# Optimization experiments

Measured on AMD Instinct MI355X. Metric: run time of the kernel, lower is better.

Reference implementation:

```python
import jax, jax.numpy as jnp
import numpy as np

B, T, V, NS, L, G, H = 16, 256, 18000, 30, 10, 3, 400


def setup_inputs() -> dict:
    key = jax.random.key(0)
    ks = jax.random.split(key, 12)
    return {
        'encoded_hidden': jax.random.normal(ks[0], (1, B, H), jnp.float32),
        'encoded_outputs': jax.random.normal(ks[1], (B, T, H), jnp.float32),
        'emb_weight': jax.random.normal(ks[2], (V, H), jnp.float32) * 0.02,
        'gru_w_ih': jax.random.normal(ks[3], (3 * H, H), jnp.float32) * 0.05,
        'gru_w_hh': jax.random.normal(ks[4], (3 * H, H), jnp.float32) * 0.05,
        'gru_b_ih': jnp.zeros((3 * H,), jnp.float32),
        'gru_b_hh': jnp.zeros((3 * H,), jnp.float32),
        'w_ratio': jax.random.normal(ks[5], (1, 3 * H), jnp.float32) * 0.05,
        'b_ratio': jnp.zeros((1,), jnp.float32),
        'w_gate': jax.random.normal(ks[6], (G, H), jnp.float32) * 0.05,
        'b_gate': jnp.zeros((G,), jnp.float32),
        'slot_emb': jax.random.normal(ks[7], (2 * NS, H), jnp.float32) * 0.1,
        'encoded_lens': jax.random.randint(ks[8], (B,), T // 2, T + 1, jnp.int32),
        'story': jax.random.randint(ks[9], (B, T), 0, V, jnp.int32),
        'target_batches': jax.random.randint(ks[10], (B, NS, L), 0, V, jnp.int32),
        'domain_idx': 2 * jnp.arange(NS, dtype=jnp.int32),
        'slotname_idx': 2 * jnp.arange(NS, dtype=jnp.int32) + 1,
    }


def _forward(encoded_hidden, encoded_outputs, emb_weight, gru_w_ih, gru_w_hh,
             gru_b_ih, gru_b_hh, w_ratio, b_ratio, w_gate, b_gate, slot_emb,
             encoded_lens, story, target_batches, domain_idx, slotname_idx):
    b, t, h = encoded_outputs.shape
    ns, l = target_batches.shape[1], target_batches.shape[2]
    n = ns * b  # flattened slot-major rows: row = slot*b + batch

    combined = slot_emb[domain_idx] + slot_emb[slotname_idx]          # (NS,H)
    dec_in0 = jnp.repeat(combined, b, axis=0)                          # (N,H)
    h0 = jnp.tile(encoded_hidden[0], (ns, 1))                          # (N,H)
    enc = jnp.tile(encoded_outputs, (ns, 1, 1))                        # (N,T,H)
    story_rep = jnp.tile(story, (ns, 1))                               # (N,T)
    lens_rep = jnp.tile(encoded_lens, ns)                              # (N,)
    mask = jnp.arange(t)[None, :] < lens_rep[:, None]                  # (N,T)
    rows = jnp.arange(n)[:, None]

    # teacher forcing: decoder input at step wi>=1 is emb of target at wi-1
    tgt = jnp.transpose(target_batches, (2, 1, 0)).reshape(l, n)       # (L,N)
    dec_inputs = jnp.concatenate([dec_in0[None], emb_weight[tgt[:-1]]], axis=0)

    def step(hid, x):
        gi = x @ gru_w_ih.T + gru_b_ih
        gh = hid @ gru_w_hh.T + gru_b_hh
        i_r, i_z, i_n = jnp.split(gi, 3, axis=-1)
        h_r, h_z, h_n = jnp.split(gh, 3, axis=-1)
        r = jax.nn.sigmoid(i_r + h_r)
        z = jax.nn.sigmoid(i_z + h_z)
        nn_ = jnp.tanh(i_n + r * h_n)
        h_new = (1.0 - z) * nn_ + z * hid                              # (N,H)
        # attend over encoder outputs
        scores = jnp.einsum('nh,nth->nt', h_new, enc)
        scores = jnp.where(mask, scores, -1e9)
        prob = jax.nn.softmax(scores, axis=1)                          # (N,T)
        context = jnp.einsum('nt,nth->nh', prob, enc)                  # (N,H)
        # vocab distribution
        p_vocab = jax.nn.softmax(h_new @ emb_weight.T, axis=1)         # (N,V)
        # pointer-generator mix
        p_gen_vec = jnp.concatenate([h_new, context, x], axis=-1)      # (N,3H)
        switch = jax.nn.sigmoid(p_gen_vec @ w_ratio.T + b_ratio)       # (N,1)
        p_ctx = jnp.zeros_like(p_vocab).at[rows, story_rep].add(prob)  # scatter-add
        final = (1.0 - switch) * p_ctx + switch * p_vocab              # (N,V)
        return h_new, (final, context)

    _, (finals, contexts) = jax.lax.scan(step, h0, dec_inputs)
    points = finals.reshape(l, ns, b, -1).transpose(1, 2, 0, 3)        # (NS,B,L,V)
    gates = (contexts[0] @ w_gate.T + b_gate).reshape(ns, b, -1)       # (NS,B,G)
    return points, gates


def reference(encoded_hidden, encoded_outputs, emb_weight, gru_w_ih, gru_w_hh,
              gru_b_ih, gru_b_hh, w_ratio, b_ratio, w_gate, b_gate, slot_emb,
              encoded_lens, story, target_batches, domain_idx, slotname_idx):
    return _forward(encoded_hidden, encoded_outputs, emb_weight, gru_w_ih,
                    gru_w_hh, gru_b_ih, gru_b_hh, w_ratio, b_ratio, w_gate,
                    b_gate, slot_emb, encoded_lens, story, target_batches,
                    domain_idx, slotname_idx)
```

## Files before the change

kernel.cpp:

```cpp
#include <hip/hip_runtime.h>
#include <hip/hip_bf16.h>

#define Bq 16
#define Tq 256
#define Vq 18000
#define NSq 30
#define Lq 10
#define Gq 3
#define Hq 400
#define Nq (NSq * Bq)
#define H3q (3 * Hq)
#define CHq 9000

typedef __bf16 bf16;
typedef __bf16 bf16x4 __attribute__((ext_vector_type(4)));
typedef __bf16 bf16x8 __attribute__((ext_vector_type(8)));
typedef float floatx16 __attribute__((ext_vector_type(16)));

__global__ __launch_bounds__(256) void k_f2b4(
    const float* __restrict__ src, bf16* __restrict__ dst, const int n4)
{
    int i = blockIdx.x * 256 + threadIdx.x;
    if (i >= n4) return;
    const float4 v = ((const float4*)src)[i];
    bf16x4 o;
    o[0] = (bf16)v.x; o[1] = (bf16)v.y; o[2] = (bf16)v.z; o[3] = (bf16)v.w;
    ((bf16x4*)dst)[i] = o;
}

__global__ __launch_bounds__(256) void k_prep(
    const float* __restrict__ slot_emb, const int* __restrict__ dom,
    const int* __restrict__ slo, const bf16* __restrict__ embb,
    const int* __restrict__ tgt, const float* __restrict__ ehid,
    float* __restrict__ h, bf16* __restrict__ hb, bf16* __restrict__ xb,
    const int step)
{
    int i = blockIdx.x * 256 + threadIdx.x;
    if (i >= Nq * Hq) return;
    int n = i / Hq, k = i - n * Hq;
    int s = n / Bq, b = n & (Bq - 1);
    if (step == 0) {
        float v = slot_emb[dom[s] * Hq + k] + slot_emb[slo[s] * Hq + k];
        xb[i] = (bf16)v;
        float hv = ehid[b * Hq + k];
        h[i] = hv;
        hb[i] = (bf16)hv;
    } else {
        int tv = tgt[(b * NSq + s) * Lq + (step - 1)];
        xb[i] = embb[(size_t)tv * Hq + k];
    }
}

__global__ __launch_bounds__(256) void k_gru_gemm(
    const bf16* __restrict__ xb, const bf16* __restrict__ hb,
    const bf16* __restrict__ w_ih, const bf16* __restrict__ w_hh,
    float* __restrict__ gi, float* __restrict__ gh)
{
    const int ct = blockIdx.x;
    const int which = blockIdx.z;
    const int wave = threadIdx.x >> 6;
    const int lane = threadIdx.x & 63;
    const int g = blockIdx.y * 4 + wave;
    if (g >= 15) return;
    const bf16* A = which ? hb : xb;
    const bf16* W = which ? w_hh : w_ih;
    float* O = which ? gh : gi;
    const int m = lane & 31;
    const int kh = (lane >> 5) * 8;
    const int row = g * 32 + m;
    int col = ct * 32 + m;
    if (col >= H3q) col = H3q - 1;
    const bf16* Ap = A + row * Hq + kh;
    const bf16* Wp = W + col * Hq + kh;
    floatx16 acc;
    #pragma unroll
    for (int r = 0; r < 16; ++r) acc[r] = 0.f;
    for (int kt = 0; kt < 25; ++kt) {
        bf16x8 a = *(const bf16x8*)(Ap + kt * 16);
        bf16x8 w = *(const bf16x8*)(Wp + kt * 16);
        acc = __builtin_amdgcn_mfma_f32_32x32x16_bf16(a, w, acc, 0, 0, 0);
    }
    const int j = ct * 32 + (lane & 31);
    if (j < H3q) {
        const int rbase = g * 32 + 4 * (lane >> 5);
        #pragma unroll
        for (int r = 0; r < 16; ++r) {
            int rr = rbase + (r & 3) + 8 * (r >> 2);
            O[rr * H3q + j] = acc[r];
        }
    }
}

__global__ __launch_bounds__(256) void k_gru_attn(
    const float* __restrict__ gi, const float* __restrict__ gh,
    const float* __restrict__ b_ih, const float* __restrict__ b_hh,
    float* __restrict__ h, bf16* __restrict__ hb,
    const bf16* __restrict__ xb, const bf16* __restrict__ encb,
    const int* __restrict__ lens, const float* __restrict__ w_ratio,
    const float* __restrict__ b_ratio, const float* __restrict__ w_gate,
    const float* __restrict__ b_gate, float* __restrict__ prob,
    float* __restrict__ swp, float* __restrict__ out_gates, const int step)
{
    const int n = blockIdx.x;
    const int b = n & (Bq - 1);
    const int tid = threadIdx.x;
    __shared__ float s_h[Hq];
    __shared__ float s_c[Hq];
    __shared__ float s_p[Tq];
    __shared__ float s_red[4];

    const float* gin = gi + n * H3q;
    const float* ghn = gh + n * H3q;
    for (int k = tid; k < Hq; k += 256) {
        float ir = gin[k]          + b_ih[k];
        float hr = ghn[k]          + b_hh[k];
        float iz = gin[Hq + k]     + b_ih[Hq + k];
        float hz = ghn[Hq + k]     + b_hh[Hq + k];
        float in_ = gin[2*Hq + k]  + b_ih[2*Hq + k];
        float hn_ = ghn[2*Hq + k]  + b_hh[2*Hq + k];
        float r = 1.f / (1.f + __expf(-(ir + hr)));
        float z = 1.f / (1.f + __expf(-(iz + hz)));
        float nn = tanhf(in_ + r * hn_);
        float hp = h[n * Hq + k];
        float hv = (1.f - z) * nn + z * hp;
        s_h[k] = hv;
        h[n * Hq + k] = hv;
        hb[n * Hq + k] = (bf16)hv;
    }
    __syncthreads();

    const int t = tid;
    const bf16* erow = encb + (size_t)(b * Tq + t) * Hq;
    float sc = 0.f;
    #pragma unroll 5
    for (int kc = 0; kc < Hq / 8; ++kc) {
        bf16x8 e = *(const bf16x8*)(erow + kc * 8);
        #pragma unroll
        for (int j = 0; j < 8; ++j) sc += s_h[kc * 8 + j] * (float)e[j];
    }
    const int len = lens[b];
    float score = (t < len) ? sc : -1e9f;

    float mx = score;
    for (int off = 32; off > 0; off >>= 1) mx = fmaxf(mx, __shfl_xor(mx, off, 64));
    if ((tid & 63) == 0) s_red[tid >> 6] = mx;
    __syncthreads();
    mx = fmaxf(fmaxf(s_red[0], s_red[1]), fmaxf(s_red[2], s_red[3]));
    float ev = __expf(score - mx);
    float sm = ev;
    for (int off = 32; off > 0; off >>= 1) sm += __shfl_xor(sm, off, 64);
    __syncthreads();
    if ((tid & 63) == 0) s_red[tid >> 6] = sm;
    __syncthreads();
    sm = s_red[0] + s_red[1] + s_red[2] + s_red[3];
    float p = ev / sm;
    s_p[t] = p;
    prob[n * Tq + t] = p;
    __syncthreads();

    for (int k = tid; k < Hq; k += 256) {
        float c = 0.f;
        const bf16* ecol = encb + (size_t)b * Tq * Hq + k;
        for (int tt = 0; tt < Tq; ++tt) c += s_p[tt] * (float)ecol[tt * Hq];
        s_c[k] = c;
    }
    __syncthreads();

    float part = 0.f;
    for (int k = tid; k < Hq; k += 256) {
        part += w_ratio[k]        * s_h[k]
              + w_ratio[Hq + k]   * s_c[k]
              + w_ratio[2*Hq + k] * (float)xb[n * Hq + k];
    }
    for (int off = 32; off > 0; off >>= 1) part += __shfl_xor(part, off, 64);
    __syncthreads();
    if ((tid & 63) == 0) s_red[tid >> 6] = part;
    __syncthreads();
    if (tid == 0) {
        float tot = s_red[0] + s_red[1] + s_red[2] + s_red[3] + b_ratio[0];
        swp[n] = 1.f / (1.f + __expf(-tot));
    }

    if (step == 0) {
        for (int gg = 0; gg < Gq; ++gg) {
            float pg = 0.f;
            for (int k = tid; k < Hq; k += 256)
                pg += w_gate[gg * Hq + k] * s_c[k];
            for (int off = 32; off > 0; off >>= 1) pg += __shfl_xor(pg, off, 64);
            __syncthreads();
            if ((tid & 63) == 0) s_red[tid >> 6] = pg;
            __syncthreads();
            if (tid == 0)
                out_gates[n * Gq + gg] =
                    s_red[0] + s_red[1] + s_red[2] + s_red[3] + b_gate[gg];
        }
    }
}

__global__ __launch_bounds__(256) void k_vocab_gemm(
    const bf16* __restrict__ hb, const bf16* __restrict__ embb,
    float* __restrict__ logits)
{
    const int ct = blockIdx.x;
    const int wave = threadIdx.x >> 6;
    const int lane = threadIdx.x & 63;
    const int m = lane & 31;
    const int kh = (lane >> 5) * 8;
    int col = ct * 32 + m;
    if (col >= Vq) col = Vq - 1;
    const bf16* Ep = embb + (size_t)col * Hq + kh;
    floatx16 acc[4];
    #pragma unroll
    for (int i = 0; i < 4; ++i)
        #pragma unroll
        for (int r = 0; r < 16; ++r) acc[i][r] = 0.f;

    for (int kt = 0; kt < 25; ++kt) {
        bf16x8 e = *(const bf16x8*)(Ep + kt * 16);
        #pragma unroll
        for (int i = 0; i < 4; ++i) {
            int g = wave + 4 * i;
            if (g < 15) {
                bf16x8 a = *(const bf16x8*)(hb + (g * 32 + m) * Hq + kh + kt * 16);
                acc[i] = __builtin_amdgcn_mfma_f32_32x32x16_bf16(a, e, acc[i], 0, 0, 0);
            }
        }
    }
    const int j = ct * 32 + (lane & 31);
    if (j < Vq) {
        #pragma unroll
        for (int i = 0; i < 4; ++i) {
            int g = wave + 4 * i;
            if (g < 15) {
                const int rbase = g * 32 + 4 * (lane >> 5);
                #pragma unroll
                for (int r = 0; r < 16; ++r) {
                    int rr = rbase + (r & 3) + 8 * (r >> 2);
                    logits[(size_t)rr * Vq + j] = acc[i][r];
                }
            }
        }
    }
}

__global__ __launch_bounds__(512) void k_softmax_final(
    const float* __restrict__ logits, const float* __restrict__ prob,
    const float* __restrict__ swp, const int* __restrict__ story,
    float* __restrict__ out, const int step)
{
    __shared__ float s_chunk[CHq];
    __shared__ float s_red[8];
    __shared__ float s_red2[8];
    __shared__ float s_MS[2];
    const int n = blockIdx.x;
    const int b = n & (Bq - 1);
    const int tid = threadIdx.x;
    const float* lr = logits + (size_t)n * Vq;

    float m = -1e30f, s = 0.f;
    for (int v = tid; v < Vq; v += 512) {
        float x = lr[v];
        float nm = fmaxf(m, x);
        s = s * __expf(m - nm) + __expf(x - nm);
        m = nm;
    }
    for (int off = 32; off > 0; off >>= 1) {
        float om = __shfl_xor(m, off, 64);
        float os = __shfl_xor(s, off, 64);
        float nm = fmaxf(m, om);
        s = s * __expf(m - nm) + os * __expf(om - nm);
        m = nm;
    }
    if ((tid & 63) == 0) { s_red[tid >> 6] = m; s_red2[tid >> 6] = s; }
    __syncthreads();
    if (tid == 0) {
        float M = -1e30f;
        for (int i = 0; i < 8; ++i) M = fmaxf(M, s_red[i]);
        float S = 0.f;
        for (int i = 0; i < 8; ++i) S += s_red2[i] * __expf(s_red[i] - M);
        s_MS[0] = M; s_MS[1] = S;
    }
    __syncthreads();
    const float M = s_MS[0];
    const float swv = swp[n];
    const float scale = swv / s_MS[1];
    float* orow = out + ((size_t)n * Lq + step) * Vq;

    #pragma unroll
    for (int c = 0; c < 2; ++c) {
        const int c0 = c * CHq;
        for (int v = tid; v < CHq; v += 512)
            s_chunk[v] = __expf(lr[c0 + v] - M) * scale;
        __syncthreads();
        if (tid < Tq) {
            int idx = story[b * Tq + tid];
            if (idx >= c0 && idx < c0 + CHq) {
                float add = (1.f - swv) * prob[n * Tq + tid];
                atomicAdd(&s_chunk[idx - c0], add);
            }
        }
        __syncthreads();
        for (int v = tid; v < CHq; v += 512)
            orow[c0 + v] = s_chunk[v];
        __syncthreads();
    }
}

extern "C" void kernel_launch(void* const* d_in, const int* in_sizes, int n_in,
                              void* d_out, int out_size, void* d_ws, size_t ws_size,
                              hipStream_t stream)
{
    const float* ehid    = (const float*)d_in[0];
    const float* enc     = (const float*)d_in[1];
    const float* emb     = (const float*)d_in[2];
    const float* w_ih    = (const float*)d_in[3];
    const float* w_hh    = (const float*)d_in[4];
    const float* b_ih    = (const float*)d_in[5];
    const float* b_hh    = (const float*)d_in[6];
    const float* w_ratio = (const float*)d_in[7];
    const float* b_ratio = (const float*)d_in[8];
    const float* w_gate  = (const float*)d_in[9];
    const float* b_gate  = (const float*)d_in[10];
    const float* slot_emb= (const float*)d_in[11];
    const int*  lens     = (const int*)d_in[12];
    const int*  story    = (const int*)d_in[13];
    const int*  tgt      = (const int*)d_in[14];
    const int*  dom      = (const int*)d_in[15];
    const int*  slo      = (const int*)d_in[16];

    float* out = (float*)d_out;
    float* out_gates = out + (size_t)NSq * Bq * Lq * Vq;

    char* w = (char*)d_ws;
    size_t off = 0;
    auto alloc = [&](size_t bytes) -> void* {
        void* p = (void*)(w + off);
        off += (bytes + 255) & ~(size_t)255;
        return p;
    };
    bf16*  xb     = (bf16*)alloc((size_t)Nq * Hq * 2);
    bf16*  hb     = (bf16*)alloc((size_t)Nq * Hq * 2);
    float* h      = (float*)alloc((size_t)Nq * Hq * 4);
    float* gi     = (float*)alloc((size_t)Nq * H3q * 4);
    float* gh     = (float*)alloc((size_t)Nq * H3q * 4);
    float* prob   = (float*)alloc((size_t)Nq * Tq * 4);
    float* swp    = (float*)alloc((size_t)Nq * 4);
    float* logits = (float*)alloc((size_t)Nq * Vq * 4);
    bf16*  embb   = (bf16*)alloc((size_t)Vq * Hq * 2);
    bf16*  wbih   = (bf16*)alloc((size_t)H3q * Hq * 2);
    bf16*  wbhh   = (bf16*)alloc((size_t)H3q * Hq * 2);
    bf16*  encb   = (bf16*)alloc((size_t)Bq * Tq * Hq * 2);

    {
        int n4;
        n4 = (Vq * Hq) / 4;
        k_f2b4<<<dim3((n4 + 255) / 256), dim3(256), 0, stream>>>(emb, embb, n4);
        n4 = (H3q * Hq) / 4;
        k_f2b4<<<dim3((n4 + 255) / 256), dim3(256), 0, stream>>>(w_ih, wbih, n4);
        k_f2b4<<<dim3((n4 + 255) / 256), dim3(256), 0, stream>>>(w_hh, wbhh, n4);
        n4 = (Bq * Tq * Hq) / 4;
        k_f2b4<<<dim3((n4 + 255) / 256), dim3(256), 0, stream>>>(enc, encb, n4);
    }

    for (int step = 0; step < Lq; ++step) {
        k_prep<<<dim3((Nq * Hq + 255) / 256), dim3(256), 0, stream>>>(
            slot_emb, dom, slo, embb, tgt, ehid, h, hb, xb, step);
        k_gru_gemm<<<dim3(38, 4, 2), dim3(256), 0, stream>>>(
            xb, hb, wbih, wbhh, gi, gh);
        k_gru_attn<<<dim3(Nq), dim3(256), 0, stream>>>(
            gi, gh, b_ih, b_hh, h, hb, xb, encb, lens, w_ratio, b_ratio,
            w_gate, b_gate, prob, swp, out_gates, step);
        k_vocab_gemm<<<dim3(563), dim3(256), 0, stream>>>(hb, embb, logits);
        k_softmax_final<<<dim3(Nq), dim3(512), 0, stream>>>(
            logits, prob, swp, story, out, step);
    }
}
```

Baseline: 1.384 ms.

## Pack MFMA operands, precompute input gates, fuse exp/rowsum into vocab GEMM

New measurement: 3.280 ms. 2.37x slower.

```diff
diff --git a/kernel.cpp b/kernel.cpp
--- a/kernel.cpp
+++ b/kernel.cpp
@@ -10,7 +10,10 @@
 #define Hq 400
 #define Nq (NSq * Bq)
 #define H3q (3 * Hq)
-#define CHq 9000
+#define NKT 25
+#define NGV 564
+#define NGW 38
+#define NGH 15
 
 typedef __bf16 bf16;
 typedef __bf16 bf16x4 __attribute__((ext_vector_type(4)));
@@ -28,74 +31,159 @@
     ((bf16x4*)dst)[i] = o;
 }
 
-__global__ __launch_bounds__(256) void k_prep(
+__global__ __launch_bounds__(256) void k_packf(
+    const float* __restrict__ src, bf16* __restrict__ dst,
+    const int ngroups, const int nrows)
+{
+    const int i = blockIdx.x * 256 + threadIdx.x;
+    if (i >= ngroups * NKT * 64) return;
+    const int lane = i & 63;
+    const int kt = (i >> 6) % NKT;
+    const int g = i / (NKT * 64);
+    int row = g * 32 + (lane & 31);
+    if (row >= nrows) row = nrows - 1;
+    const int k0 = kt * 16 + (lane >> 5) * 8;
+    const float* s = src + (size_t)row * Hq + k0;
+    const float4 a = *(const float4*)s;
+    const float4 c = *(const float4*)(s + 4);
+    bf16x8 o;
+    o[0] = (bf16)a.x; o[1] = (bf16)a.y; o[2] = (bf16)a.z; o[3] = (bf16)a.w;
+    o[4] = (bf16)c.x; o[5] = (bf16)c.y; o[6] = (bf16)c.z; o[7] = (bf16)c.w;
+    *(bf16x8*)(dst + (size_t)i * 8) = o;
+}
+
+__global__ __launch_bounds__(256) void k_xball(
     const float* __restrict__ slot_emb, const int* __restrict__ dom,
-    const int* __restrict__ slo, const bf16* __restrict__ embb,
-    const int* __restrict__ tgt, const float* __restrict__ ehid,
-    float* __restrict__ h, bf16* __restrict__ hb, bf16* __restrict__ xb,
-    const int step)
-{
-    int i = blockIdx.x * 256 + threadIdx.x;
-    if (i >= Nq * Hq) return;
-    int n = i / Hq, k = i - n * Hq;
-    int s = n / Bq, b = n & (Bq - 1);
-    if (step == 0) {
-        float v = slot_emb[dom[s] * Hq + k] + slot_emb[slo[s] * Hq + k];
-        xb[i] = (bf16)v;
-        float hv = ehid[b * Hq + k];
-        h[i] = hv;
-        hb[i] = (bf16)hv;
+    const int* __restrict__ slo, const float* __restrict__ emb,
+    const int* __restrict__ tgt, bf16* __restrict__ xbp,
+    bf16* __restrict__ xlin)
+{
+    const int i = blockIdx.x * 256 + threadIdx.x;
+    if (i >= Lq * NGH * NKT * 64) return;
+    const int lane = i & 63;
+    const int kt = (i >> 6) % NKT;
+    const int gg = i / (NKT * 64);
+    const int g = gg % NGH;
+    const int s = gg / NGH;
+    const int n = g * 32 + (lane & 31);
+    const int slot = n >> 4, b = n & (Bq - 1);
+    const int k0 = kt * 16 + (lane >> 5) * 8;
+    float v[8];
+    if (s == 0) {
+        const float* p1 = slot_emb + (size_t)dom[slot] * Hq + k0;
+        const float* p2 = slot_emb + (size_t)slo[slot] * Hq + k0;
+        #pragma unroll
+        for (int j = 0; j < 8; ++j) v[j] = p1[j] + p2[j];
     } else {
-        int tv = tgt[(b * NSq + s) * Lq + (step - 1)];
-        xb[i] = embb[(size_t)tv * Hq + k];
-    }
-}
-
-__global__ __launch_bounds__(256) void k_gru_gemm(
-    const bf16* __restrict__ xb, const bf16* __restrict__ hb,
-    const bf16* __restrict__ w_ih, const bf16* __restrict__ w_hh,
-    float* __restrict__ gi, float* __restrict__ gh)
+        const int tv = tgt[(b * NSq + slot) * Lq + (s - 1)];
+        const float* p = emb + (size_t)tv * Hq + k0;
+        #pragma unroll
+        for (int j = 0; j < 8; ++j) v[j] = p[j];
+    }
+    bf16x8 o;
+    #pragma unroll
+    for (int j = 0; j < 8; ++j) o[j] = (bf16)v[j];
+    *(bf16x8*)(xbp + (size_t)i * 8) = o;
+    *(bf16x8*)(xlin + ((size_t)(s * Nq + n)) * Hq + k0) = o;
+}
+
+__global__ __launch_bounds__(256) void k_h0(
+    const float* __restrict__ ehid, float* __restrict__ h,
+    bf16* __restrict__ hbp)
+{
+    const int i = blockIdx.x * 256 + threadIdx.x;
+    if (i >= NGH * NKT * 64) return;
+    const int lane = i & 63;
+    const int kt = (i >> 6) % NKT;
+    const int g = i / (NKT * 64);
+    const int n = g * 32 + (lane & 31);
+    const int b = n & (Bq - 1);
+    const int k0 = kt * 16 + (lane >> 5) * 8;
+    const float* s = ehid + (size_t)b * Hq + k0;
+    bf16x8 o;
+    #pragma unroll
+    for (int j = 0; j < 8; ++j) {
+        float v = s[j];
+        h[(size_t)n * Hq + k0 + j] = v;
+        o[j] = (bf16)v;
+    }
+    *(bf16x8*)(hbp + (size_t)i * 8) = o;
+}
+
+__global__ __launch_bounds__(256) void k_gi_all(
+    const bf16* __restrict__ xbp, const bf16* __restrict__ wihp,
+    float* __restrict__ gi_all)
 {
     const int ct = blockIdx.x;
-    const int which = blockIdx.z;
-    const int wave = threadIdx.x >> 6;
-    const int lane = threadIdx.x & 63;
+    const int s = blockIdx.y;
+    const int wave = threadIdx.x >> 6, lane = threadIdx.x & 63;
+    floatx16 acc[4];
+    #pragma unroll
+    for (int i = 0; i < 4; ++i)
+        #pragma unroll
+        for (int r = 0; r < 16; ++r) acc[i][r] = 0.f;
+    for (int kt = 0; kt < NKT; ++kt) {
+        const bf16x8 w = *(const bf16x8*)(wihp + ((size_t)(ct * NKT + kt) * 64 + lane) * 8);
+        #pragma unroll
+        for (int i = 0; i < 4; ++i) {
+            const int g = wave + 4 * i;
+            if (g < NGH) {
+                const bf16x8 a = *(const bf16x8*)(xbp +
+                    ((size_t)((s * NGH + g) * NKT + kt) * 64 + lane) * 8);
+                acc[i] = __builtin_amdgcn_mfma_f32_32x32x16_bf16(a, w, acc[i], 0, 0, 0);
+            }
+        }
+    }
+    const int j = ct * 32 + (lane & 31);
+    if (j >= H3q) return;
+    #pragma unroll
+    for (int i = 0; i < 4; ++i) {
+        const int g = wave + 4 * i;
+        if (g < NGH) {
+            const int rbase = g * 32 + 4 * (lane >> 5);
+            #pragma unroll
+            for (int r = 0; r < 16; ++r) {
+                const int rr = rbase + (r & 3) + 8 * (r >> 2);
+                gi_all[((size_t)(s * Nq + rr)) * H3q + j] = acc[i][r];
+            }
+        }
+    }
+}
+
+__global__ __launch_bounds__(256) void k_gh(
+    const bf16* __restrict__ hbp, const bf16* __restrict__ whhp,
+    float* __restrict__ gh, float* __restrict__ rowsum)
+{
+    if (blockIdx.x == 0 && blockIdx.y == 0) {
+        for (int v = threadIdx.x; v < Nq; v += 256) rowsum[v] = 0.f;
+    }
+    const int ct = blockIdx.x;
+    const int wave = threadIdx.x >> 6, lane = threadIdx.x & 63;
     const int g = blockIdx.y * 4 + wave;
-    if (g >= 15) return;
-    const bf16* A = which ? hb : xb;
-    const bf16* W = which ? w_hh : w_ih;
-    float* O = which ? gh : gi;
-    const int m = lane & 31;
-    const int kh = (lane >> 5) * 8;
-    const int row = g * 32 + m;
-    int col = ct * 32 + m;
-    if (col >= H3q) col = H3q - 1;
-    const bf16* Ap = A + row * Hq + kh;
-    const bf16* Wp = W + col * Hq + kh;
+    if (g >= NGH) return;
     floatx16 acc;
     #pragma unroll
     for (int r = 0; r < 16; ++r) acc[r] = 0.f;
-    for (int kt = 0; kt < 25; ++kt) {
-        bf16x8 a = *(const bf16x8*)(Ap + kt * 16);
-        bf16x8 w = *(const bf16x8*)(Wp + kt * 16);
+    for (int kt = 0; kt < NKT; ++kt) {
+        const bf16x8 a = *(const bf16x8*)(hbp + ((size_t)(g * NKT + kt) * 64 + lane) * 8);
+        const bf16x8 w = *(const bf16x8*)(whhp + ((size_t)(ct * NKT + kt) * 64 + lane) * 8);
         acc = __builtin_amdgcn_mfma_f32_32x32x16_bf16(a, w, acc, 0, 0, 0);
     }
     const int j = ct * 32 + (lane & 31);
-    if (j < H3q) {
-        const int rbase = g * 32 + 4 * (lane >> 5);
-        #pragma unroll
-        for (int r = 0; r < 16; ++r) {
-            int rr = rbase + (r & 3) + 8 * (r >> 2);
-            O[rr * H3q + j] = acc[r];
-        }
-    }
-}
-
-__global__ __launch_bounds__(256) void k_gru_attn(
-    const float* __restrict__ gi, const float* __restrict__ gh,
+    if (j >= H3q) return;
+    const int rbase = g * 32 + 4 * (lane >> 5);
+    #pragma unroll
+    for (int r = 0; r < 16; ++r) {
+        const int rr = rbase + (r & 3) + 8 * (r >> 2);
+        gh[(size_t)rr * H3q + j] = acc[r];
+    }
+}
+
+__global__ __launch_bounds__(256) void k_attn(
+    const float* __restrict__ gi_all, const float* __restrict__ gh,
     const float* __restrict__ b_ih, const float* __restrict__ b_hh,
-    float* __restrict__ h, bf16* __restrict__ hb,
-    const bf16* __restrict__ xb, const bf16* __restrict__ encb,
+    float* __restrict__ h, bf16* __restrict__ hbp,
+    const bf16* __restrict__ xlin, const bf16* __restrict__ encb,
     const int* __restrict__ lens, const float* __restrict__ w_ratio,
     const float* __restrict__ b_ratio, const float* __restrict__ w_gate,
     const float* __restrict__ b_gate, float* __restrict__ prob,
@@ -109,8 +197,8 @@
     __shared__ float s_p[Tq];
     __shared__ float s_red[4];
 
-    const float* gin = gi + n * H3q;
-    const float* ghn = gh + n * H3q;
+    const float* gin = gi_all + ((size_t)step * Nq + n) * H3q;
+    const float* ghn = gh + (size_t)n * H3q;
     for (int k = tid; k < Hq; k += 256) {
         float ir = gin[k]          + b_ih[k];
         float hr = ghn[k]          + b_hh[k];
@@ -121,26 +209,40 @@
         float r = 1.f / (1.f + __expf(-(ir + hr)));
         float z = 1.f / (1.f + __expf(-(iz + hz)));
         float nn = tanhf(in_ + r * hn_);
-        float hp = h[n * Hq + k];
+        float hp = h[(size_t)n * Hq + k];
         float hv = (1.f - z) * nn + z * hp;
         s_h[k] = hv;
-        h[n * Hq + k] = hv;
-        hb[n * Hq + k] = (bf16)hv;
-    }
-    __syncthreads();
-
-    const int t = tid;
-    const bf16* erow = encb + (size_t)(b * Tq + t) * Hq;
-    float sc = 0.f;
-    #pragma unroll 5
-    for (int kc = 0; kc < Hq / 8; ++kc) {
-        bf16x8 e = *(const bf16x8*)(erow + kc * 8);
-        #pragma unroll
-        for (int j = 0; j < 8; ++j) sc += s_h[kc * 8 + j] * (float)e[j];
-    }
+        h[(size_t)n * Hq + k] = hv;
+        hbp[((size_t)(((n >> 5) * NKT + (k >> 4)) * 64
+                      + ((k >> 3) & 1) * 32 + (n & 31))) * 8 + (k & 7)] = (bf16)hv;
+    }
+    __syncthreads();
+
+    const int lane = tid & 63;
+    const int wv = tid >> 6;
+    float hreg[8];
+    #pragma unroll
+    for (int j = 0; j < 8; ++j) hreg[j] = 0.f;
+    if (lane < 50) {
+        #pragma unroll
+        for (int j = 0; j < 8; ++j) hreg[j] = s_h[lane * 8 + j];
+    }
+    for (int it = 0; it < 64; ++it) {
+        const int t = wv * 64 + it;
+        float part = 0.f;
+        if (lane < 50) {
+            const bf16x8 e = *(const bf16x8*)(encb + ((size_t)(b * Tq + t)) * Hq + lane * 8);
+            #pragma unroll
+            for (int j = 0; j < 8; ++j) part += hreg[j] * (float)e[j];
+        }
+        #pragma unroll
+        for (int off = 32; off > 0; off >>= 1) part += __shfl_xor(part, off, 64);
+        if (lane == 0) s_p[t] = part;
+    }
+    __syncthreads();
+
     const int len = lens[b];
-    float score = (t < len) ? sc : -1e9f;
-
+    float score = (tid < len) ? s_p[tid] : -1e9f;
     float mx = score;
     for (int off = 32; off > 0; off >>= 1) mx = fmaxf(mx, __shfl_xor(mx, off, 64));
     if ((tid & 63) == 0) s_red[tid >> 6] = mx;
@@ -154,27 +256,28 @@
     __syncthreads();
     sm = s_red[0] + s_red[1] + s_red[2] + s_red[3];
     float p = ev / sm;
-    s_p[t] = p;
-    prob[n * Tq + t] = p;
+    s_p[tid] = p;
+    prob[n * Tq + tid] = p;
     __syncthreads();
 
     for (int k = tid; k < Hq; k += 256) {
         float c = 0.f;
         const bf16* ecol = encb + (size_t)b * Tq * Hq + k;
-        for (int tt = 0; tt < Tq; ++tt) c += s_p[tt] * (float)ecol[tt * Hq];
+        for (int tt = 0; tt < Tq; ++tt) c += s_p[tt] * (float)ecol[(size_t)tt * Hq];
         s_c[k] = c;
     }
     __syncthreads();
 
-    float part = 0.f;
+    const bf16* xr = xlin + ((size_t)step * Nq + n) * Hq;
+    float part2 = 0.f;
     for (int k = tid; k < Hq; k += 256) {
-        part += w_ratio[k]        * s_h[k]
-              + w_ratio[Hq + k]   * s_c[k]
-              + w_ratio[2*Hq + k] * (float)xb[n * Hq + k];
-    }
-    for (int off = 32; off > 0; off >>= 1) part += __shfl_xor(part, off, 64);
-    __syncthreads();
-    if ((tid & 63) == 0) s_red[tid >> 6] = part;
+        part2 += w_ratio[k]        * s_h[k]
+               + w_ratio[Hq + k]   * s_c[k]
+               + w_ratio[2*Hq + k] * (float)xr[k];
+    }
+    for (int off = 32; off > 0; off >>= 1) part2 += __shfl_xor(part2, off, 64);
+    __syncthreads();
+    if ((tid & 63) == 0) s_red[tid >> 6] = part2;
     __syncthreads();
     if (tid == 0) {
         float tot = s_red[0] + s_red[1] + s_red[2] + s_red[3] + b_ratio[0];
@@ -197,112 +300,85 @@
     }
 }
 
-__global__ __launch_bounds__(256) void k_vocab_gemm(
-    const bf16* __restrict__ hb, const bf16* __restrict__ embb,
-    float* __restrict__ logits)
-{
-    const int ct = blockIdx.x;
-    const int wave = threadIdx.x >> 6;
-    const int lane = threadIdx.x & 63;
-    const int m = lane & 31;
-    const int kh = (lane >> 5) * 8;
-    int col = ct * 32 + m;
-    if (col >= Vq) col = Vq - 1;
-    const bf16* Ep = embb + (size_t)col * Hq + kh;
-    floatx16 acc[4];
+__global__ __launch_bounds__(256, 2) void k_vocab(
+    const bf16* __restrict__ hbp, const bf16* __restrict__ embp,
+    float* __restrict__ eL, float* __restrict__ rowsum)
+{
+    const int ct2 = blockIdx.x;
+    const int wave = threadIdx.x >> 6, lane = threadIdx.x & 63;
+    floatx16 acc0[4], acc1[4];
     #pragma unroll
     for (int i = 0; i < 4; ++i)
         #pragma unroll
-        for (int r = 0; r < 16; ++r) acc[i][r] = 0.f;
-
-    for (int kt = 0; kt < 25; ++kt) {
-        bf16x8 e = *(const bf16x8*)(Ep + kt * 16);
+        for (int r = 0; r < 16; ++r) { acc0[i][r] = 0.f; acc1[i][r] = 0.f; }
+
+    for (int kt = 0; kt < NKT; ++kt) {
+        const bf16x8 w0 = *(const bf16x8*)(embp +
+            ((size_t)((2 * ct2) * NKT + kt) * 64 + lane) * 8);
+        const bf16x8 w1 = *(const bf16x8*)(embp +
+            ((size_t)((2 * ct2 + 1) * NKT + kt) * 64 + lane) * 8);
         #pragma unroll
         for (int i = 0; i < 4; ++i) {
-            int g = wave + 4 * i;
-            if (g < 15) {
-                bf16x8 a = *(const bf16x8*)(hb + (g * 32 + m) * Hq + kh + kt * 16);
-                acc[i] = __builtin_amdgcn_mfma_f32_32x32x16_bf16(a, e, acc[i], 0, 0, 0);
+            const int g = wave + 4 * i;
+            if (g < NGH) {
+                const bf16x8 a = *(const bf16x8*)(hbp +
+                    ((size_t)(g * NKT + kt) * 64 + lane) * 8);
+                acc0[i] = __builtin_amdgcn_mfma_f32_32x32x16_bf16(a, w0, acc0[i], 0, 0, 0);
+                acc1[i] = __builtin_amdgcn_mfma_f32_32x32x16_bf16(a, w1, acc1[i], 0, 0, 0);
             }
         }
     }
-    const int j = ct * 32 + (lane & 31);
-    if (j < Vq) {
-        #pragma unroll
-        for (int i = 0; i < 4; ++i) {
-            int g = wave + 4 * i;
-            if (g < 15) {
-                const int rbase = g * 32 + 4 * (lane >> 5);
-                #pragma unroll
-                for (int r = 0; r < 16; ++r) {
-                    int rr = rbase + (r & 3) + 8 * (r >> 2);
-                    logits[(size_t)rr * Vq + j] = acc[i][r];
-                }
-            }
-        }
-    }
-}
-
-__global__ __launch_bounds__(512) void k_softmax_final(
-    const float* __restrict__ logits, const float* __restrict__ prob,
-    const float* __restrict__ swp, const int* __restrict__ story,
-    float* __restrict__ out, const int step)
-{
-    __shared__ float s_chunk[CHq];
-    __shared__ float s_red[8];
-    __shared__ float s_red2[8];
-    __shared__ float s_MS[2];
+
+    const int mcol = lane & 31, half = lane >> 5;
+    const int j0 = ct2 * 64 + mcol, j1 = j0 + 32;
+    #pragma unroll
+    for (int i = 0; i < 4; ++i) {
+        const int g = wave + 4 * i;
+        if (g >= NGH) continue;
+        const int rbase = g * 32 + 4 * half;
+        #pragma unroll
+        for (int r = 0; r < 16; ++r) {
+            const int rr = rbase + (r & 3) + 8 * (r >> 2);
+            const float e0 = (j0 < Vq) ? __expf(acc0[i][r]) : 0.f;
+            const float e1 = (j1 < Vq) ? __expf(acc1[i][r]) : 0.f;
+            if (j0 < Vq) eL[(size_t)rr * Vq + j0] = e0;
+            if (j1 < Vq) eL[(size_t)rr * Vq + j1] = e1;
+            float v = e0 + e1;
+            v += __shfl_xor(v, 16, 64);
+            v += __shfl_xor(v, 8, 64);
+            v += __shfl_xor(v, 4, 64);
+            v += __shfl_xor(v, 2, 64);
+            v += __shfl_xor(v, 1, 64);
+            if (mcol == 0) atomicAdd(&rowsum[rr], v);
+        }
+    }
+}
+
+__global__ __launch_bounds__(512) void k_final(
+    const float* __restrict__ eL, const float* __restrict__ prob,
+    const float* __restrict__ swp, const float* __restrict__ rowsum,
+    const int* __restrict__ story, float* __restrict__ out, const int step)
+{
     const int n = blockIdx.x;
     const int b = n & (Bq - 1);
     const int tid = threadIdx.x;
-    const float* lr = logits + (size_t)n * Vq;
-
-    float m = -1e30f, s = 0.f;
-    for (int v = tid; v < Vq; v += 512) {
-        float x = lr[v];
-        float nm = fmaxf(m, x);
-        s = s * __expf(m - nm) + __expf(x - nm);
-        m = nm;
-    }
-    for (int off = 32; off > 0; off >>= 1) {
-        float om = __shfl_xor(m, off, 64);
-        float os = __shfl_xor(s, off, 64);
-        float nm = fmaxf(m, om);
-        s = s * __expf(m - nm) + os * __expf(om - nm);
-        m = nm;
-    }
-    if ((tid & 63) == 0) { s_red[tid >> 6] = m; s_red2[tid >> 6] = s; }
-    __syncthreads();
-    if (tid == 0) {
-        float M = -1e30f;
-        for (int i = 0; i < 8; ++i) M = fmaxf(M, s_red[i]);
-        float S = 0.f;
-        for (int i = 0; i < 8; ++i) S += s_red2[i] * __expf(s_red[i] - M);
-        s_MS[0] = M; s_MS[1] = S;
-    }
-    __syncthreads();
-    const float M = s_MS[0];
     const float swv = swp[n];
-    const float scale = swv / s_MS[1];
+    const float scale = swv / rowsum[n];
+    const float4* e4 = (const float4*)(eL + (size_t)n * Vq);
     float* orow = out + ((size_t)n * Lq + step) * Vq;
-
-    #pragma unroll
-    for (int c = 0; c < 2; ++c) {
-        const int c0 = c * CHq;
-        for (int v = tid; v < CHq; v += 512)
-            s_chunk[v] = __expf(lr[c0 + v] - M) * scale;
-        __syncthreads();
-        if (tid < Tq) {
-            int idx = story[b * Tq + tid];
-            if (idx >= c0 && idx < c0 + CHq) {
-                float add = (1.f - swv) * prob[n * Tq + tid];
-                atomicAdd(&s_chunk[idx - c0], add);
-            }
-        }
-        __syncthreads();
-        for (int v = tid; v < CHq; v += 512)
-            orow[c0 + v] = s_chunk[v];
-        __syncthreads();
+    float4* o4 = (float4*)orow;
+    for (int v = tid; v < Vq / 4; v += 512) {
+        const float4 e = e4[v];
+        float4 o;
+        o.x = e.x * scale; o.y = e.y * scale;
+        o.z = e.z * scale; o.w = e.w * scale;
+        o4[v] = o;
+    }
+    __syncthreads();
+    __threadfence();
+    if (tid < Tq) {
+        const int idx = story[b * Tq + tid];
+        atomicAdd(orow + idx, (1.f - swv) * prob[n * Tq + tid]);
     }
 }
 
@@ -338,40 +414,45 @@
         off += (bytes + 255) & ~(size_t)255;
         return p;
     };
-    bf16*  xb     = (bf16*)alloc((size_t)Nq * Hq * 2);
-    bf16*  hb     = (bf16*)alloc((size_t)Nq * Hq * 2);
+    bf16*  xbp    = (bf16*)alloc((size_t)Lq * Nq * Hq * 2);
+    bf16*  xlin   = (bf16*)alloc((size_t)Lq * Nq * Hq * 2);
+    bf16*  hbp    = (bf16*)alloc((size_t)Nq * Hq * 2);
     float* h      = (float*)alloc((size_t)Nq * Hq * 4);
-    float* gi     = (float*)alloc((size_t)Nq * H3q * 4);
+    float* gi_all = (float*)alloc((size_t)Lq * Nq * H3q * 4);
     float* gh     = (float*)alloc((size_t)Nq * H3q * 4);
     float* prob   = (float*)alloc((size_t)Nq * Tq * 4);
     float* swp    = (float*)alloc((size_t)Nq * 4);
-    float* logits = (float*)alloc((size_t)Nq * Vq * 4);
-    bf16*  embb   = (bf16*)alloc((size_t)Vq * Hq * 2);
-    bf16*  wbih   = (bf16*)alloc((size_t)H3q * Hq * 2);
-    bf16*  wbhh   = (bf16*)alloc((size_t)H3q * Hq * 2);
+    float* rowsum = (float*)alloc((size_t)Nq * 4);
+    float* eL     = (float*)alloc((size_t)Nq * Vq * 4);
+    bf16*  embp   = (bf16*)alloc((size_t)NGV * NKT * 64 * 8 * 2);
+    bf16*  wihp   = (bf16*)alloc((size_t)NGW * NKT * 64 * 8 * 2);
+    bf16*  whhp   = (bf16*)alloc((size_t)NGW * NKT * 64 * 8 * 2);
     bf16*  encb   = (bf16*)alloc((size_t)Bq * Tq * Hq * 2);
 
     {
-        int n4;
-        n4 = (Vq * Hq) / 4;
-        k_f2b4<<<dim3((n4 + 255) / 256), dim3(256), 0, stream>>>(emb, embb, n4);
-        n4 = (H3q * Hq) / 4;
-        k_f2b4<<<dim3((n4 + 255) / 256), dim3(256), 0, stream>>>(w_ih, wbih, n4);
-        k_f2b4<<<dim3((n4 + 255) / 256), dim3(256), 0, stream>>>(w_hh, wbhh, n4);
-        n4 = (Bq * Tq * Hq) / 4;
+        int nf;
+        nf = NGV * NKT * 64;
+        k_packf<<<dim3((nf + 255) / 256), dim3(256), 0, stream>>>(emb, embp, NGV, Vq);
+        nf = NGW * NKT * 64;
+        k_packf<<<dim3((nf + 255) / 256), dim3(256), 0, stream>>>(w_ih, wihp, NGW, H3q);
+        k_packf<<<dim3((nf + 255) / 256), dim3(256), 0, stream>>>(w_hh, whhp, NGW, H3q);
+        const int n4 = (Bq * Tq * Hq) / 4;
         k_f2b4<<<dim3((n4 + 255) / 256), dim3(256), 0, stream>>>(enc, encb, n4);
+        nf = Lq * NGH * NKT * 64;
+        k_xball<<<dim3((nf + 255) / 256), dim3(256), 0, stream>>>(
+            slot_emb, dom, slo, emb, tgt, xbp, xlin);
+        nf = NGH * NKT * 64;
+        k_h0<<<dim3((nf + 255) / 256), dim3(256), 0, stream>>>(ehid, h, hbp);
+        k_gi_all<<<dim3(NGW, Lq), dim3(256), 0, stream>>>(xbp, wihp, gi_all);
     }
 
     for (int step = 0; step < Lq; ++step) {
-        k_prep<<<dim3((Nq * Hq + 255) / 256), dim3(256), 0, stream>>>(
-            slot_emb, dom, slo, embb, tgt, ehid, h, hb, xb, step);
-        k_gru_gemm<<<dim3(38, 4, 2), dim3(256), 0, stream>>>(
-            xb, hb, wbih, wbhh, gi, gh);
-        k_gru_attn<<<dim3(Nq), dim3(256), 0, stream>>>(
-            gi, gh, b_ih, b_hh, h, hb, xb, encb, lens, w_ratio, b_ratio,
+        k_gh<<<dim3(NGW, 4), dim3(256), 0, stream>>>(hbp, whhp, gh, rowsum);
+        k_attn<<<dim3(Nq), dim3(256), 0, stream>>>(
+            gi_all, gh, b_ih, b_hh, h, hbp, xlin, encb, lens, w_ratio, b_ratio,
             w_gate, b_gate, prob, swp, out_gates, step);
-        k_vocab_gemm<<<dim3(563), dim3(256), 0, stream>>>(hb, embb, logits);
-        k_softmax_final<<<dim3(Nq), dim3(512), 0, stream>>>(
-            logits, prob, swp, story, out, step);
-    }
-}
+        k_vocab<<<dim3(282), dim3(256), 0, stream>>>(hbp, embp, eL, rowsum);
+        k_final<<<dim3(Nq), dim3(512), 0, stream>>>(
+            eL, prob, swp, rowsum, story, out, step);
+    }
+}
```
